# Kernel optimization log

Measured on AMD Instinct MI355X. Metric: run time of the kernel, lower is better.

Reference implementation:

```python
import jax, jax.numpy as jnp
import numpy as np

T = 4096        # teams (HC nodes)
N_COORD = 3     # coordinators per team (OC, SC, DC)
N_POS = 32      # position coaches per coordinator
NPT = 1 + N_COORD + N_COORD * N_POS   # 100 nodes per team
N = T * NPT     # 409600 total nodes
IN_DIM = 128
EMB = 64


def _build_indices():
    base = np.arange(T, dtype=np.int32) * NPT
    hc_ids = base                                                    # [T]
    coord = base[:, None] + 1 + np.arange(N_COORD, dtype=np.int32)   # [T,3]
    pos = (base[:, None, None] + 1 + N_COORD
           + (np.arange(N_COORD, dtype=np.int32) * N_POS)[None, :, None]
           + np.arange(N_POS, dtype=np.int32)[None, None, :])        # [T,3,32]
    src1 = np.broadcast_to(coord[:, :, None], (T, N_COORD, N_POS)).reshape(-1)
    tgt1 = pos.reshape(-1)
    src2 = np.repeat(base, N_COORD)
    tgt2 = coord.reshape(-1)
    return (jnp.asarray(src1), jnp.asarray(tgt1),
            jnp.asarray(src2), jnp.asarray(tgt2), jnp.asarray(hc_ids))


def setup_inputs() -> dict:
    key = jax.random.key(0)
    k = jax.random.split(key, 5)
    src1, tgt1, src2, tgt2, hc_ids = _build_indices()
    gain = 1.414  # relu gain, xavier_normal-style scale
    f = jax.random.normal(k[0], (N, IN_DIM), jnp.float32)
    salary = jax.random.normal(k[1], (T, 1), jnp.float32)
    W_fc = jax.random.normal(k[2], (EMB, IN_DIM), jnp.float32) * gain * (2.0 / (IN_DIM + EMB)) ** 0.5
    W_attn = jax.random.normal(k[3], (1, 2 * EMB), jnp.float32) * gain * (2.0 / (2 * EMB + 1)) ** 0.5
    b_attn = jnp.zeros((1,), jnp.float32)
    W_out = jax.random.normal(k[4], (2, EMB + 1), jnp.float32) * gain * (2.0 / (EMB + 1 + 2)) ** 0.5
    b_out = jnp.zeros((2,), jnp.float32)
    return {"f": f, "salary": salary, "W_fc": W_fc, "W_attn": W_attn,
            "b_attn": b_attn, "W_out": W_out, "b_out": b_out,
            "src1": src1, "tgt1": tgt1, "src2": src2, "tgt2": tgt2,
            "hc_ids": hc_ids}


def _segment_softmax(e, seg, num_segments):
    m = jax.ops.segment_max(e, seg, num_segments=num_segments)
    ex = jnp.exp(e - m[seg])
    denom = jax.ops.segment_sum(ex, seg, num_segments=num_segments)
    return ex / denom[seg]


def _gat_level(z, src, tgt, W_attn, b_attn):
    # per-edge attention logit: leaky_relu(attn_fc([z_src, z_tgt]))
    z2 = jnp.concatenate([z[src], z[tgt]], axis=1)          # [E, 2*EMB]
    e = jax.nn.leaky_relu(z2 @ W_attn.T + b_attn)[:, 0]     # [E]
    alpha = _segment_softmax(e, src, N)                     # softmax over edges grouped by source
    agg = jax.ops.segment_sum(alpha[:, None] * z[tgt], src, num_segments=N)
    has_edge = jax.ops.segment_sum(jnp.ones_like(e), src, num_segments=N) > 0
    # only source nodes get their z replaced by relu(weighted sum)
    return jnp.where(has_edge[:, None], jax.nn.relu(agg), z)


def reference(f, salary, W_fc, W_attn, b_attn, W_out, b_out,
              src1, tgt1, src2, tgt2, hc_ids):
    z = jax.nn.relu(f @ W_fc.T)                             # [N, EMB]
    z = _gat_level(z, src1, tgt1, W_attn, b_attn)           # coord <- positions
    z = _gat_level(z, src2, tgt2, W_attn, b_attn)           # hc <- coords
    team_emb = z[hc_ids]                                    # [T, EMB]
    h = jnp.concatenate([team_emb, salary], axis=1)         # [T, EMB+1]
    y = jax.nn.relu(h @ W_out.T + b_out)                    # [T, 2]
    return jax.nn.softmax(y, axis=1)
```

## Files before the change

### kernel.cpp

```cpp
#include <hip/hip_runtime.h>

typedef short v8s __attribute__((ext_vector_type(8)));
typedef float v4f __attribute__((ext_vector_type(4)));
typedef unsigned int v4u __attribute__((ext_vector_type(4)));
typedef unsigned int v2u __attribute__((ext_vector_type(2)));

#define NPT 100
#define IN_DIM 128
#define FMAXO 209715184u

__device__ __forceinline__ unsigned int cvt_pk(float x0, float x1) {
    unsigned int r;
    asm("v_cvt_pk_bf16_f32 %0, %1, %2" : "=v"(r) : "v"(x0), "v"(x1));
    return r;
}
__device__ __forceinline__ float bflo(unsigned int u) { return __uint_as_float(u << 16); }
__device__ __forceinline__ float bfhi(unsigned int u) { return __uint_as_float(u & 0xffff0000u); }

union ABfrag { v8s v; v4u u; };

__device__ __forceinline__ ABfrag pack8(float4 x0, float4 x1) {
    ABfrag r;
    r.u[0] = cvt_pk(x0.x, x0.y);
    r.u[1] = cvt_pk(x0.z, x0.w);
    r.u[2] = cvt_pk(x1.x, x1.y);
    r.u[3] = cvt_pk(x1.z, x1.w);
    return r;
}

#define ISSUE(BUF, TBOFF) do {                                                   \
    _Pragma("unroll") for (int i_ = 0; i_ < 8; ++i_) {                           \
        unsigned o_ = (TBOFF) + i_ * 1024u + lane16;                             \
        o_ = o_ < FMAXO ? o_ : FMAXO;                                            \
        BUF[i_] = *(const v4f*)(fbytes + o_);                                    \
    }                                                                            \
} while (0)

#define TSTORE(LT, BUF) do {                                                     \
    _Pragma("unroll") for (int i_ = 0; i_ < 8; ++i_) {                           \
        const int row_ = 2 * i_ + (lane >> 5);                                   \
        unsigned b_ = (unsigned)(row_ * 256 + (lane & 31) * 8);                  \
        b_ ^= (unsigned)((row_ & 7) << 4);                                       \
        v2u w_;                                                                  \
        w_.x = cvt_pk(BUF[i_].x, BUF[i_].y);                                     \
        w_.y = cvt_pk(BUF[i_].z, BUF[i_].w);                                     \
        *(v2u*)((LT) + b_) = w_;                                                 \
    }                                                                            \
} while (0)

#define CONSUME(T, LT) do {                                                      \
    v4f acc_[4] = {{0,0,0,0},{0,0,0,0},{0,0,0,0},{0,0,0,0}};                     \
    _Pragma("unroll") for (int ks_ = 0; ks_ < 4; ++ks_) {                        \
        const unsigned rb_ = (unsigned)(l15 * 256 + ks_ * 64 + g * 16)           \
                           ^ (unsigned)((l15 & 7) << 4);                         \
        v8s fr_ = *(const v8s*)((LT) + rb_);                                     \
        _Pragma("unroll") for (int n_ = 0; n_ < 4; ++n_) {                       \
            v8s bh_ = *(const v8s*)&wl[(ks_ * 256 + n_ * 64 + lane) * 8];        \
            acc_[n_] = __builtin_amdgcn_mfma_f32_16x16x32_bf16(fr_, bh_, acc_[n_], 0, 0, 0); \
        }                                                                        \
    }                                                                            \
    const bool live_ = ((T) < 6) || (g == 0);                                    \
    float zr_[4][4];                                                             \
    _Pragma("unroll") for (int n_ = 0; n_ < 4; ++n_)                             \
        _Pragma("unroll") for (int j_ = 0; j_ < 4; ++j_)                         \
            zr_[n_][j_] = live_ ? fmaxf(acc_[n_][j_], 0.f) : 0.f;                \
    _Pragma("unroll") for (int n_ = 0; n_ < 4; ++n_) {                           \
        zp[T][n_][0] = cvt_pk(zr_[n_][0], zr_[n_][1]);                           \
        zp[T][n_][1] = cvt_pk(zr_[n_][2], zr_[n_][3]);                           \
    }                                                                            \
    const bool useL_ = ((T) == 0) && (g == 0);            \
    _Pragma("unroll") for (int j_ = 0; j_ < 4; ++j_) {                           \
        float d_ = (useL_ ? aLv[0] : aRv[0]) * zr_[0][j_]                        \
                 + (useL_ ? aLv[1] : aRv[1]) * zr_[1][j_]                        \
                 + (useL_ ? aLv[2] : aRv[2]) * zr_[2][j_]                        \
                 + (useL_ ? aLv[3] : aRv[3]) * zr_[3][j_];                       \
        d_ += __shfl_xor(d_, 8, 64); d_ += __shfl_xor(d_, 4, 64);                \
        d_ += __shfl_xor(d_, 2, 64); d_ += __shfl_xor(d_, 1, 64);                \
        const int r_ = 16 * (T) + 4 * g + j_;                                    \
        if (l15 == j_ && ((T) < 6 || r_ < NPT)) sDa[r_] = d_;                    \
    }                                                                            \
} while (0)

#define TAIL(TEAMI) do {                                                         \
    {                       \
        const int c_ = lane >> 5, p_ = lane & 31;                                \
        float e_ = sDa[1 + c_] + sDa[4 + 32 * c_ + p_] + bA;                     \
        e_ = e_ > 0.f ? e_ : 0.01f * e_;                                         \
        float mx_ = e_;                                                          \
        mx_ = fmaxf(mx_, __shfl_xor(mx_, 16, 64)); mx_ = fmaxf(mx_, __shfl_xor(mx_, 8, 64)); \
        mx_ = fmaxf(mx_, __shfl_xor(mx_, 4, 64));  mx_ = fmaxf(mx_, __shfl_xor(mx_, 2, 64)); \
        mx_ = fmaxf(mx_, __shfl_xor(mx_, 1, 64));                                \
        float ex_ = __expf(e_ - mx_), sm_ = ex_;                                 \
        sm_ += __shfl_xor(sm_, 16, 64); sm_ += __shfl_xor(sm_, 8, 64);           \
        sm_ += __shfl_xor(sm_, 4, 64);  sm_ += __shfl_xor(sm_, 2, 64);           \
        sm_ += __shfl_xor(sm_, 1, 64);                                           \
        sDa[4 + lane] = ex_ / sm_;                                               \
    }                                                                            \
    if (lane < 32) {                                                \
        float e_ = sDa[3] + sDa[68 + lane] + bA;                                 \
        e_ = e_ > 0.f ? e_ : 0.01f * e_;                                         \
        float mx_ = e_;                                                          \
        mx_ = fmaxf(mx_, __shfl_xor(mx_, 16, 64)); mx_ = fmaxf(mx_, __shfl_xor(mx_, 8, 64)); \
        mx_ = fmaxf(mx_, __shfl_xor(mx_, 4, 64));  mx_ = fmaxf(mx_, __shfl_xor(mx_, 2, 64)); \
        mx_ = fmaxf(mx_, __shfl_xor(mx_, 1, 64));                                \
        float ex_ = __expf(e_ - mx_), sm_ = ex_;                                 \
        sm_ += __shfl_xor(sm_, 16, 64); sm_ += __shfl_xor(sm_, 8, 64);           \
        sm_ += __shfl_xor(sm_, 4, 64);  sm_ += __shfl_xor(sm_, 2, 64);           \
        sm_ += __shfl_xor(sm_, 1, 64);                                           \
        sDa[68 + lane] = ex_ / sm_;                                              \
    }                                                                            \
    float zn_[3][4], sRn_[3];                                                    \
    _Pragma("unroll") for (int c_ = 0; c_ < 3; ++c_) {                           \
        float s_[4] = {0.f, 0.f, 0.f, 0.f};                                      \
        _Pragma("unroll") for (int ti_ = 0; ti_ < 3; ++ti_) {                    \
            const int T_ = 2 * c_ + ti_;                                         \
            float4 av_ = *(const float4*)&sDa[16 * T_ + 4 * g];                  \
            const float msk_ = (ti_ == 0) ? (g >= 1 ? 1.f : 0.f)                 \
                             : (ti_ == 2) ? (g == 0 ? 1.f : 0.f) : 1.f;          \
            av_.x *= msk_; av_.y *= msk_; av_.z *= msk_; av_.w *= msk_;          \
            _Pragma("unroll") for (int n_ = 0; n_ < 4; ++n_) {                   \
                s_[n_] += av_.x * bflo(zp[T_][n_][0]) + av_.y * bfhi(zp[T_][n_][0]) \
                        + av_.z * bflo(zp[T_][n_][1]) + av_.w * bfhi(zp[T_][n_][1]); \
            }                                                                    \
        }                                                                        \
        _Pragma("unroll") for (int n_ = 0; n_ < 4; ++n_) {                       \
            s_[n_] += __shfl_xor(s_[n_], 16, 64);                                \
            s_[n_] += __shfl_xor(s_[n_], 32, 64);                                \
            zn_[c_][n_] = fmaxf(s_[n_], 0.f);                                    \
        }                                                                        \
        float pr_ = aRv[0] * zn_[c_][0] + aRv[1] * zn_[c_][1]                    \
                  + aRv[2] * zn_[c_][2] + aRv[3] * zn_[c_][3];                   \
        pr_ += __shfl_xor(pr_, 8, 64); pr_ += __shfl_xor(pr_, 4, 64);            \
        pr_ += __shfl_xor(pr_, 2, 64); pr_ += __shfl_xor(pr_, 1, 64);            \
        sRn_[c_] = pr_;                                                          \
    }                                                                            \
    {                                                                            \
        const float s0_ = sDa[0];                                                \
        float e0_ = s0_ + sRn_[0] + bA; e0_ = e0_ > 0.f ? e0_ : 0.01f * e0_;     \
        float e1_ = s0_ + sRn_[1] + bA; e1_ = e1_ > 0.f ? e1_ : 0.01f * e1_;     \
        float e2_ = s0_ + sRn_[2] + bA; e2_ = e2_ > 0.f ? e2_ : 0.01f * e2_;     \
        const float mx_ = fmaxf(e0_, fmaxf(e1_, e2_));                           \
        const float x0_ = __expf(e0_ - mx_), x1_ = __expf(e1_ - mx_), x2_ = __expf(e2_ - mx_); \
        const float inv_ = 1.f / (x0_ + x1_ + x2_);                              \
        float p0_ = 0.f, p1_ = 0.f;                                              \
        _Pragma("unroll") for (int n_ = 0; n_ < 4; ++n_) {                       \
            const float zh_ = fmaxf((x0_ * zn_[0][n_] + x1_ * zn_[1][n_]         \
                                   + x2_ * zn_[2][n_]) * inv_, 0.f);             \
            p0_ += W_out[n_ * 16 + l15] * zh_;                                   \
            p1_ += W_out[65 + n_ * 16 + l15] * zh_;                              \
        }                                                                        \
        p0_ += __shfl_xor(p0_, 8, 64); p0_ += __shfl_xor(p0_, 4, 64);            \
        p0_ += __shfl_xor(p0_, 2, 64); p0_ += __shfl_xor(p0_, 1, 64);            \
        p1_ += __shfl_xor(p1_, 8, 64); p1_ += __shfl_xor(p1_, 4, 64);            \
        p1_ += __shfl_xor(p1_, 2, 64); p1_ += __shfl_xor(p1_, 1, 64);            \
        if (lane == 0) {                                                         \
            const float sal_ = salary[TEAMI];                                    \
            float y0_ = fmaxf(p0_ + W_out[64]  * sal_ + b_out[0], 0.f);          \
            float y1_ = fmaxf(p1_ + W_out[129] * sal_ + b_out[1], 0.f);          \
            const float mm_ = fmaxf(y0_, y1_);                                   \
            const float q0_ = __expf(y0_ - mm_), q1_ = __expf(y1_ - mm_);        \
            const float is_ = 1.f / (q0_ + q1_);                                 \
            out[(TEAMI) * 2 + 0] = q0_ * is_;                                    \
            out[(TEAMI) * 2 + 1] = q1_ * is_;                                    \
        }                                                                        \
    }                                                                            \
} while (0)

__global__ __launch_bounds__(256, 2) void wteam2_kernel(
    const float* __restrict__ f, const float* __restrict__ salary,
    const float* __restrict__ W_fc, const float* __restrict__ W_attn,
    const float* __restrict__ b_attn, const float* __restrict__ W_out,
    const float* __restrict__ b_out, float* __restrict__ out)
{
    __shared__ __align__(16) unsigned short wl[8192];
    __shared__ __align__(16) char lt_all[4][2][4096];
    __shared__ __align__(16) float sD_all[4][112];

    const int tid  = threadIdx.x;
    const int lane = tid & 63;
    const int wave = tid >> 6;
    const int l15  = lane & 15;
    const int g    = lane >> 4;
    const unsigned lane16 = (unsigned)lane * 16u;
    float* sDa = sD_all[wave];
    char* LT0 = lt_all[wave][0];
    char* LT1 = lt_all[wave][1];
    const char* fbytes = (const char*)f;

    #pragma unroll
    for (int i = 0; i < 4; ++i) {
        const int s = i * 256 + tid;
        const int ks = s >> 8, nt = (s >> 6) & 3, sl = s & 63;
        const float* src = W_fc + (nt * 16 + (sl & 15)) * IN_DIM + ks * 32 + 8 * (sl >> 4);
        ABfrag wv = pack8(*(const float4*)src, *(const float4*)(src + 4));
        *(v4u*)&wl[s * 8] = wv.u;
    }

    float aLv[4], aRv[4];
    #pragma unroll
    for (int n = 0; n < 4; ++n) {
        aLv[n] = W_attn[n * 16 + l15];
        aRv[n] = W_attn[64 + n * 16 + l15];
    }
    const float bA = b_attn[0];
    if (lane < 12) sDa[100 + lane] = 0.f;

    const size_t team0 = ((size_t)blockIdx.x * 4 + wave) * 2;
    const unsigned tb0 = (unsigned)team0 * 51200u;
    const unsigned tb1 = tb0 + 51200u;

    __syncthreads();

    v4f R0[8], R1[8];
    unsigned int zp[7][4][2];

    ISSUE(R0, tb0 + 0 * 8192u);
    ISSUE(R1, tb0 + 1 * 8192u);
    TSTORE(LT0, R0);
    ISSUE(R0, tb0 + 2 * 8192u); TSTORE(LT1, R1); CONSUME(0, LT0);
    ISSUE(R1, tb0 + 3 * 8192u); TSTORE(LT0, R0); CONSUME(1, LT1);
    ISSUE(R0, tb0 + 4 * 8192u); TSTORE(LT1, R1); CONSUME(2, LT0);
    ISSUE(R1, tb0 + 5 * 8192u); TSTORE(LT0, R0); CONSUME(3, LT1);
    ISSUE(R0, tb0 + 6 * 8192u); TSTORE(LT1, R1); CONSUME(4, LT0);
    ISSUE(R1, tb1 + 0 * 8192u); TSTORE(LT0, R0); CONSUME(5, LT1);
    ISSUE(R0, tb1 + 1 * 8192u); TSTORE(LT1, R1); CONSUME(6, LT0);
    TAIL(team0);
    ISSUE(R1, tb1 + 2 * 8192u); TSTORE(LT0, R0); CONSUME(0, LT1);
    ISSUE(R0, tb1 + 3 * 8192u); TSTORE(LT1, R1); CONSUME(1, LT0);
    ISSUE(R1, tb1 + 4 * 8192u); TSTORE(LT0, R0); CONSUME(2, LT1);
    ISSUE(R0, tb1 + 5 * 8192u); TSTORE(LT1, R1); CONSUME(3, LT0);
    ISSUE(R1, tb1 + 6 * 8192u); TSTORE(LT0, R0); CONSUME(4, LT1);
    TSTORE(LT1, R1); CONSUME(5, LT0);
    CONSUME(6, LT1);
    TAIL(team0 + 1);
}

extern "C" void kernel_launch(void* const* d_in, const int* in_sizes, int n_in,
                              void* d_out, int out_size, void* d_ws, size_t ws_size,
                              hipStream_t stream) {
    const float* f      = (const float*)d_in[0];
    const float* salary = (const float*)d_in[1];
    const float* W_fc   = (const float*)d_in[2];
    const float* W_attn = (const float*)d_in[3];
    const float* b_attn = (const float*)d_in[4];
    const float* W_out  = (const float*)d_in[5];
    const float* b_out  = (const float*)d_in[6];
    wteam2_kernel<<<dim3(512), dim3(256), 0, stream>>>(
        f, salary, W_fc, W_attn, b_attn, W_out, b_out, (float*)d_out);
}
```

Baseline: 42.72 us.

## Pair tile consumption to interleave two MFMA chains per LDS round

Restructures the per-wave software pipeline so two 16-row tiles are loaded into LDS and then consumed together. Their MFMA chains are interleaved, sharing each weight fragment load, with two global loads in flight per phase. This is meant to hide MFMA dependency latency and halve the weight-fragment LDS reads. In exchange it raises register pressure from the doubled accumulators and coarsens the load/compute overlap pattern.

Measured after the change: 43.18 us. No clear change (+1.1%).

```diff
diff --git a/kernel.cpp b/kernel.cpp
--- a/kernel.cpp
+++ b/kernel.cpp
@@ -48,22 +48,12 @@
     }                                                                            \
 } while (0)
 
-#define CONSUME(T, LT) do {                                                      \
-    v4f acc_[4] = {{0,0,0,0},{0,0,0,0},{0,0,0,0},{0,0,0,0}};                     \
-    _Pragma("unroll") for (int ks_ = 0; ks_ < 4; ++ks_) {                        \
-        const unsigned rb_ = (unsigned)(l15 * 256 + ks_ * 64 + g * 16)           \
-                           ^ (unsigned)((l15 & 7) << 4);                         \
-        v8s fr_ = *(const v8s*)((LT) + rb_);                                     \
-        _Pragma("unroll") for (int n_ = 0; n_ < 4; ++n_) {                       \
-            v8s bh_ = *(const v8s*)&wl[(ks_ * 256 + n_ * 64 + lane) * 8];        \
-            acc_[n_] = __builtin_amdgcn_mfma_f32_16x16x32_bf16(fr_, bh_, acc_[n_], 0, 0, 0); \
-        }                                                                        \
-    }                                                                            \
+#define CONSPOST(T, ACC) do {                                                    \
     const bool live_ = ((T) < 6) || (g == 0);                                    \
     float zr_[4][4];                                                             \
     _Pragma("unroll") for (int n_ = 0; n_ < 4; ++n_)                             \
         _Pragma("unroll") for (int j_ = 0; j_ < 4; ++j_)                         \
-            zr_[n_][j_] = live_ ? fmaxf(acc_[n_][j_], 0.f) : 0.f;                \
+            zr_[n_][j_] = live_ ? fmaxf(ACC[n_][j_], 0.f) : 0.f;                 \
     _Pragma("unroll") for (int n_ = 0; n_ < 4; ++n_) {                           \
         zp[T][n_][0] = cvt_pk(zr_[n_][0], zr_[n_][1]);                           \
         zp[T][n_][1] = cvt_pk(zr_[n_][2], zr_[n_][3]);                           \
@@ -79,6 +69,38 @@
         const int r_ = 16 * (T) + 4 * g + j_;                                    \
         if (l15 == j_ && ((T) < 6 || r_ < NPT)) sDa[r_] = d_;                    \
     }                                                                            \
+} while (0)
+
+#define CONSUME2(TA, LTA, TB, LTB) do {                                          \
+    v4f aA_[4] = {{0,0,0,0},{0,0,0,0},{0,0,0,0},{0,0,0,0}};                      \
+    v4f aB_[4] = {{0,0,0,0},{0,0,0,0},{0,0,0,0},{0,0,0,0}};                      \
+    _Pragma("unroll") for (int ks_ = 0; ks_ < 4; ++ks_) {                        \
+        const unsigned rb_ = (unsigned)(l15 * 256 + ks_ * 64 + g * 16)           \
+                           ^ (unsigned)((l15 & 7) << 4);                         \
+        v8s frA_ = *(const v8s*)((LTA) + rb_);                                   \
+        v8s frB_ = *(const v8s*)((LTB) + rb_);                                   \
+        _Pragma("unroll") for (int n_ = 0; n_ < 4; ++n_) {                       \
+            v8s bh_ = *(const v8s*)&wl[(ks_ * 256 + n_ * 64 + lane) * 8];        \
+            aA_[n_] = __builtin_amdgcn_mfma_f32_16x16x32_bf16(frA_, bh_, aA_[n_], 0, 0, 0); \
+            aB_[n_] = __builtin_amdgcn_mfma_f32_16x16x32_bf16(frB_, bh_, aB_[n_], 0, 0, 0); \
+        }                                                                        \
+    }                                                                            \
+    CONSPOST(TA, aA_);                                                           \
+    CONSPOST(TB, aB_);                                                           \
+} while (0)
+
+#define CONSUME(T, LT) do {                                                      \
+    v4f acc_[4] = {{0,0,0,0},{0,0,0,0},{0,0,0,0},{0,0,0,0}};                     \
+    _Pragma("unroll") for (int ks_ = 0; ks_ < 4; ++ks_) {                        \
+        const unsigned rb_ = (unsigned)(l15 * 256 + ks_ * 64 + g * 16)           \
+                           ^ (unsigned)((l15 & 7) << 4);                         \
+        v8s fr_ = *(const v8s*)((LT) + rb_);                                     \
+        _Pragma("unroll") for (int n_ = 0; n_ < 4; ++n_) {                       \
+            v8s bh_ = *(const v8s*)&wl[(ks_ * 256 + n_ * 64 + lane) * 8];        \
+            acc_[n_] = __builtin_amdgcn_mfma_f32_16x16x32_bf16(fr_, bh_, acc_[n_], 0, 0, 0); \
+        }                                                                        \
+    }                                                                            \
+    CONSPOST(T, acc_);                                                           \
 } while (0)
 
 #define TAIL(TEAMI) do {                                                         \
@@ -217,20 +239,30 @@
     ISSUE(R0, tb0 + 0 * 8192u);
     ISSUE(R1, tb0 + 1 * 8192u);
     TSTORE(LT0, R0);
-    ISSUE(R0, tb0 + 2 * 8192u); TSTORE(LT1, R1); CONSUME(0, LT0);
-    ISSUE(R1, tb0 + 3 * 8192u); TSTORE(LT0, R0); CONSUME(1, LT1);
-    ISSUE(R0, tb0 + 4 * 8192u); TSTORE(LT1, R1); CONSUME(2, LT0);
-    ISSUE(R1, tb0 + 5 * 8192u); TSTORE(LT0, R0); CONSUME(3, LT1);
-    ISSUE(R0, tb0 + 6 * 8192u); TSTORE(LT1, R1); CONSUME(4, LT0);
-    ISSUE(R1, tb1 + 0 * 8192u); TSTORE(LT0, R0); CONSUME(5, LT1);
-    ISSUE(R0, tb1 + 1 * 8192u); TSTORE(LT1, R1); CONSUME(6, LT0);
+    TSTORE(LT1, R1);
+    ISSUE(R0, tb0 + 2 * 8192u); ISSUE(R1, tb0 + 3 * 8192u);
+    CONSUME2(0, LT0, 1, LT1);
+    TSTORE(LT0, R0); TSTORE(LT1, R1);
+    ISSUE(R0, tb0 + 4 * 8192u); ISSUE(R1, tb0 + 5 * 8192u);
+    CONSUME2(2, LT0, 3, LT1);
+    TSTORE(LT0, R0); TSTORE(LT1, R1);
+    ISSUE(R0, tb0 + 6 * 8192u); ISSUE(R1, tb1 + 0 * 8192u);
+    CONSUME2(4, LT0, 5, LT1);
+    TSTORE(LT0, R0); TSTORE(LT1, R1);
+    ISSUE(R0, tb1 + 1 * 8192u);
+    CONSUME(6, LT0);
     TAIL(team0);
-    ISSUE(R1, tb1 + 2 * 8192u); TSTORE(LT0, R0); CONSUME(0, LT1);
-    ISSUE(R0, tb1 + 3 * 8192u); TSTORE(LT1, R1); CONSUME(1, LT0);
-    ISSUE(R1, tb1 + 4 * 8192u); TSTORE(LT0, R0); CONSUME(2, LT1);
-    ISSUE(R0, tb1 + 5 * 8192u); TSTORE(LT1, R1); CONSUME(3, LT0);
-    ISSUE(R1, tb1 + 6 * 8192u); TSTORE(LT0, R0); CONSUME(4, LT1);
-    TSTORE(LT1, R1); CONSUME(5, LT0);
+    TSTORE(LT0, R0);
+
+    ISSUE(R0, tb1 + 2 * 8192u); ISSUE(R1, tb1 + 3 * 8192u);
+    CONSUME2(0, LT1, 1, LT0);
+    TSTORE(LT1, R0); TSTORE(LT0, R1);
+    ISSUE(R0, tb1 + 4 * 8192u); ISSUE(R1, tb1 + 5 * 8192u);
+    CONSUME2(2, LT1, 3, LT0);
+    TSTORE(LT1, R0); TSTORE(LT0, R1);
+    ISSUE(R0, tb1 + 6 * 8192u);
+    CONSUME2(4, LT1, 5, LT0);
+    TSTORE(LT1, R0);
     CONSUME(6, LT1);
     TAIL(team0 + 1);
 }
```
